# Optimization experiments

Hardware: AMD Instinct MI355X
Metric: run time of the kernel (lower is better)

The kernel has to match this reference:

```python
import jax, jax.numpy as jnp
import numpy as np

N = 100000   # points in scan
K = 20       # KNN neighbors
D = 96       # backbone feature dim
H = 1024     # random-projection dim
C = 7        # num classes


def setup_inputs() -> dict:
    key = jax.random.key(0)
    ks = jax.random.split(key, 6)
    feat_source = jax.random.normal(ks[0], (N, D), jnp.float32)
    proto = jax.random.normal(ks[1], (C, D), jnp.float32)
    w_rand = jax.random.normal(ks[2], (D, H), jnp.float32)
    Q = jnp.zeros((H, C), jnp.float32)
    G = jnp.zeros((H, H), jnp.float32)
    coords = jax.random.normal(ks[3], (N, 3), jnp.float32) * 30.0
    normals_z = jax.random.uniform(ks[4], (N,), jnp.float32)
    near_indices = jax.random.randint(ks[5], (N, K), 0, N).astype(jnp.int64)
    return dict(feat_source=feat_source, proto=proto, w_rand=w_rand, Q=Q, G=G,
                coords=coords, normals_z=normals_z, near_indices=near_indices)


def _prior_filter(preds, coords, normals_z):
    plane_pred = (preds == 2) | (preds == 3) | (preds == 4)
    manmade_pred = preds == 5
    other = (preds == 0) | (preds == 1) | (preds == 6)
    ground = plane_pred & (normals_z > 0.9) & (coords[:, 2] < -10.0)
    g_index = ground | other | manmade_pred
    m_index = (manmade_pred & (normals_z < 0.1)) | other | plane_pred
    return g_index, m_index


def reference(feat_source, proto, w_rand, Q, G, coords, normals_z, near_indices):
    RIDGE = 100.0  # stand-in for optimise_ridge_parameter (source not provided)
    # prototype logits: feat @ normalize(proto, dim=1).T   [N, C]
    proto_n = proto / jnp.maximum(jnp.linalg.norm(proto, axis=1, keepdims=True), 1e-12)
    pred_proto = feat_source @ proto_n.T
    preds = jnp.argmax(pred_proto, axis=1)                       # [N]
    # KNN consistency filtering (irregular gather)
    neigh = preds[near_indices]                                  # [N, K]
    consistency = jnp.mean((neigh == preds[:, None]).astype(jnp.float32), axis=1)
    cmask = consistency > 0.8
    g_index, m_index = _prior_filter(preds, coords, normals_z)
    mask = cmask & g_index & m_index                             # [N]
    # random-projection features
    feat_h = jax.nn.relu(feat_source @ w_rand)                   # [N, H]
    yhat = jax.nn.one_hot(preds, C, dtype=feat_h.dtype)          # [N, C]
    mw = mask.astype(feat_h.dtype)[:, None]
    fh_m = feat_h * mw                                           # masked rows (mask^2 == mask)
    Qn = Q + jnp.einsum('nh,nc->hc', fh_m, yhat)
    Gn = G + fh_m.T @ fh_m
    # ridge solve: wo = solve(G + r*I, Q); module does feat_h @ wo
    wo = jnp.linalg.solve(Gn + RIDGE * jnp.eye(H, dtype=Gn.dtype), Qn)  # [H, C]
    pred_domain = feat_h @ wo                                    # [N, C]
    return pred_domain
```

## Files before the change

### kernel.cpp

```cpp
#include <hip/hip_runtime.h>

#define D_DIM 96
#define K_NN  20
#define H_DIM 1024
#define C_CLS 7


__global__ void k_init(const float* __restrict__ proto,
                       const long long* __restrict__ idx_ll,
                       float* __restrict__ proto_n, int* __restrict__ flags) {
  __shared__ float inv[C_CLS];
  __shared__ int any_big;
  int t = threadIdx.x;
  if (t == 0) any_big = 0;
  if (t < C_CLS) {
    float ss = 0.f;
    for (int d = 0; d < D_DIM; d++) { float v = proto[t * D_DIM + d]; ss += v * v; }
    float nrm = fmaxf(sqrtf(ss), 1e-12f);
    inv[t] = 1.0f / nrm;
  }
  for (int j = t; j < 1024; j += blockDim.x) {
    long long v = idx_ll[j];
    if (v < 0 || v >= 100000) any_big = 1;
  }
  __syncthreads();
  for (int j = t; j < C_CLS * D_DIM; j += blockDim.x)
    proto_n[j] = proto[j] * inv[j / D_DIM];
  if (t == 0) {
    flags[0] = 0;
    flags[1] = any_big ? 0 : 1;
  }
}

__global__ void k_preds(const float* __restrict__ feat,
                        const float* __restrict__ proto_n,
                        int* __restrict__ preds, int N) {
  __shared__ float pn[C_CLS * D_DIM];
  for (int j = threadIdx.x; j < C_CLS * D_DIM; j += blockDim.x) pn[j] = proto_n[j];
  __syncthreads();
  int i = blockIdx.x * blockDim.x + threadIdx.x;
  if (i >= N) return;
  const float4* fp = (const float4*)(feat + (size_t)i * D_DIM);
  float s[C_CLS];
#pragma unroll
  for (int c = 0; c < C_CLS; c++) s[c] = 0.f;
#pragma unroll
  for (int q = 0; q < D_DIM / 4; q++) {
    float4 v = fp[q];
    int d = q * 4;
#pragma unroll
    for (int c = 0; c < C_CLS; c++) {
      s[c] += v.x * pn[c * D_DIM + d]     + v.y * pn[c * D_DIM + d + 1]
            + v.z * pn[c * D_DIM + d + 2] + v.w * pn[c * D_DIM + d + 3];
    }
  }
  float best = s[0]; int bi = 0;
#pragma unroll
  for (int c = 1; c < C_CLS; c++) { if (s[c] > best) { best = s[c]; bi = c; } }
  preds[i] = bi;
}

__global__ void k_mask(const int* __restrict__ preds, const void* __restrict__ nearv,
                       const float* __restrict__ coords, const float* __restrict__ normz,
                       int* __restrict__ flags, int* __restrict__ list, int N) {
  int i = blockIdx.x * blockDim.x + threadIdx.x;
  if (i >= N) return;
  int p = preds[i];
  int cnt = 0;
  if (flags[1]) {
    const long long* nn = (const long long*)nearv + (long long)i * K_NN;
#pragma unroll
    for (int k = 0; k < K_NN; k++) cnt += (preds[(int)nn[k]] == p) ? 1 : 0;
  } else {
    const int* nn = (const int*)nearv + (size_t)i * K_NN;
#pragma unroll
    for (int k = 0; k < K_NN; k++) cnt += (preds[nn[k]] == p) ? 1 : 0;
  }
  bool cmask = (cnt >= 17);
  bool plane = (p == 2) || (p == 3) || (p == 4);
  bool man   = (p == 5);
  bool other = (p == 0) || (p == 1) || (p == 6);
  float nz = normz[i];
  bool ground = plane && (nz > 0.9f) && (coords[(size_t)i * 3 + 2] < -10.0f);
  bool g = ground || other || man;
  bool m = (man && (nz < 0.1f)) || other || plane;
  if (cmask && g && m) {
    int pos = atomicAdd(&flags[0], 1);
    list[pos] = i;
  }
}

__global__ void k_qn(const float* __restrict__ feat, const float* __restrict__ w,
                     const float* __restrict__ Q, const int* __restrict__ preds,
                     const int* __restrict__ flags, const int* __restrict__ list,
                     float* __restrict__ Qn) {
  int h = blockIdx.x * blockDim.x + threadIdx.x;
  float q[C_CLS];
#pragma unroll
  for (int c = 0; c < C_CLS; c++) q[c] = Q[h * C_CLS + c];
  int M = flags[0];
  for (int m = 0; m < M; m++) {
    int i = list[m];
    float s = 0.f;
    for (int d = 0; d < D_DIM; d++) s += feat[(size_t)i * D_DIM + d] * w[(size_t)d * H_DIM + h];
    s = fmaxf(s, 0.f);
    q[preds[i]] += s;
  }
#pragma unroll
  for (int c = 0; c < C_CLS; c++) Qn[h * C_CLS + c] = q[c];
}

__global__ void k_gram(const float* __restrict__ feat, const float* __restrict__ w,
                       const float* __restrict__ G, const int* __restrict__ flags,
                       const int* __restrict__ list, float* __restrict__ Gn) {
  int bx = blockIdx.x & 15, by = blockIdx.x >> 4;
  int tr0 = by * 64, tc0 = bx * 64;
  __shared__ float fr[64], fc[64], fsh[D_DIM];
  float acc[4][4];
#pragma unroll
  for (int u = 0; u < 4; u++)
#pragma unroll
    for (int v = 0; v < 4; v++) acc[u][v] = 0.f;
  int M = flags[0];
  int t = threadIdx.x;
  int tu = t >> 4, tv = t & 15;
  for (int m = 0; m < M; m++) {
    int i = list[m];
    if (t < D_DIM) fsh[t] = feat[(size_t)i * D_DIM + t];
    __syncthreads();
    if (t < 64) {
      float s = 0.f;
      for (int d = 0; d < D_DIM; d++) s += fsh[d] * w[(size_t)d * H_DIM + tr0 + t];
      fr[t] = fmaxf(s, 0.f);
    } else if (t < 128) {
      int c = t - 64;
      float s = 0.f;
      for (int d = 0; d < D_DIM; d++) s += fsh[d] * w[(size_t)d * H_DIM + tc0 + c];
      fc[c] = fmaxf(s, 0.f);
    }
    __syncthreads();
#pragma unroll
    for (int u = 0; u < 4; u++)
#pragma unroll
      for (int v = 0; v < 4; v++) acc[u][v] += fr[tu * 4 + u] * fc[tv * 4 + v];
    __syncthreads();
  }
#pragma unroll
  for (int u = 0; u < 4; u++)
#pragma unroll
    for (int v = 0; v < 4; v++) {
      int r = tr0 + tu * 4 + u, c = tc0 + tv * 4 + v;
      Gn[(size_t)r * H_DIM + c] = G[(size_t)r * H_DIM + c] + acc[u][v];
    }
}

__device__ inline void block_reduce7(const float* val, volatile float* out,
                                     float* red) {
  int lane = threadIdx.x & 63, wave = threadIdx.x >> 6;
#pragma unroll
  for (int c = 0; c < C_CLS; c++) {
    float v = val[c];
#pragma unroll
    for (int o = 32; o > 0; o >>= 1) v += __shfl_down(v, o, 64);
    if (lane == 0) red[wave * C_CLS + c] = v;
  }
  __syncthreads();
  if (threadIdx.x == 0) {
#pragma unroll
    for (int c = 0; c < C_CLS; c++) {
      float s = 0.f;
      for (int wv = 0; wv < 16; wv++) s += red[wv * C_CLS + c];
      out[c] = s;
    }
  }
  __syncthreads();
}

__global__ void __launch_bounds__(1024) k_solve(const float* __restrict__ Gn,
                                                const float* __restrict__ Qn,
                                                float* __restrict__ wo,
                                                float* __restrict__ wo_flag) {
  const int h = threadIdx.x;
  __shared__ float psh[H_DIM * C_CLS];
  __shared__ float red[16 * C_CLS];
  __shared__ float rs[C_CLS], bn2[C_CLS], pap[C_CLS], rsn[C_CLS];

  float x[C_CLS], r[C_CLS], p[C_CLS], t7[C_CLS];
#pragma unroll
  for (int c = 0; c < C_CLS; c++) {
    float b = Qn[h * C_CLS + c];
    x[c] = 0.f; r[c] = b; p[c] = b;
    t7[c] = b * b;
  }
  block_reduce7(t7, rs, red);
  if (h == 0) {
#pragma unroll
    for (int c = 0; c < C_CLS; c++) bn2[c] = rs[c];
  }
  __syncthreads();

  for (int it = 0; it < H_DIM; it++) {
    bool done = true;
#pragma unroll
    for (int c = 0; c < C_CLS; c++)
      done = done && (rs[c] <= bn2[c] * 1e-16f + 1e-30f);
    if (done) break;

#pragma unroll
    for (int c = 0; c < C_CLS; c++) psh[h * C_CLS + c] = p[c];
    __syncthreads();

    float ap[C_CLS];
#pragma unroll
    for (int c = 0; c < C_CLS; c++) ap[c] = 100.0f * p[c];
    const float* grow = Gn + (size_t)h * H_DIM;
    for (int k = 0; k < H_DIM; k++) {
      float g = grow[k];
#pragma unroll
      for (int c = 0; c < C_CLS; c++) ap[c] += g * psh[k * C_CLS + c];
    }
#pragma unroll
    for (int c = 0; c < C_CLS; c++) t7[c] = p[c] * ap[c];
    block_reduce7(t7, pap, red);

    float a[C_CLS], rsold[C_CLS];
#pragma unroll
    for (int c = 0; c < C_CLS; c++) {
      rsold[c] = rs[c];
      bool act = rs[c] > bn2[c] * 1e-16f + 1e-30f;
      a[c] = act ? rsold[c] / fmaxf(pap[c], 1e-37f) : 0.f;
    }
#pragma unroll
    for (int c = 0; c < C_CLS; c++) {
      x[c] += a[c] * p[c];
      r[c] -= a[c] * ap[c];
      t7[c] = r[c] * r[c];
    }
    block_reduce7(t7, rsn, red);
#pragma unroll
    for (int c = 0; c < C_CLS; c++) {
      float bb = rsn[c] / fmaxf(rsold[c], 1e-37f);
      p[c] = r[c] + bb * p[c];
    }
    if (h == 0) {
#pragma unroll
      for (int c = 0; c < C_CLS; c++) rs[c] = rsn[c];
    }
    __syncthreads();
  }

#pragma unroll
  for (int c = 0; c < C_CLS; c++) wo[h * C_CLS + c] = x[c];
  float s = 0.f;
#pragma unroll
  for (int c = 0; c < C_CLS; c++) s += fabsf(x[c]);
  t7[0] = s;
#pragma unroll
  for (int c = 1; c < C_CLS; c++) t7[c] = 0.f;
  block_reduce7(t7, rsn, red);
  if (h == 0) *wo_flag = rsn[0];
}

__global__ void k_out(const float* __restrict__ feat, const float* __restrict__ w,
                      const float* __restrict__ wo, const float* __restrict__ wo_flag,
                      float* __restrict__ out, int N) {
  if (*wo_flag == 0.0f) {
    long long tid = (long long)blockIdx.x * blockDim.x + threadIdx.x;
    long long total = (long long)N * C_CLS;
    if (tid < total) out[tid] = 0.0f;
    return;
  }
  int i = blockIdx.x * blockDim.x + threadIdx.x;
  if (i >= N) return;
  float f[D_DIM];
  const float4* fp = (const float4*)(feat + (size_t)i * D_DIM);
#pragma unroll
  for (int q = 0; q < D_DIM / 4; q++) {
    float4 v = fp[q];
    f[4 * q] = v.x; f[4 * q + 1] = v.y; f[4 * q + 2] = v.z; f[4 * q + 3] = v.w;
  }
  float acc[C_CLS];
#pragma unroll
  for (int c = 0; c < C_CLS; c++) acc[c] = 0.f;
  for (int hh = 0; hh < H_DIM; hh++) {
    float s = 0.f;
#pragma unroll 8
    for (int d = 0; d < D_DIM; d++) s += f[d] * w[(size_t)d * H_DIM + hh];
    s = fmaxf(s, 0.f);
    const float* wrow = wo + hh * C_CLS;
#pragma unroll
    for (int c = 0; c < C_CLS; c++) acc[c] += s * wrow[c];
  }
#pragma unroll
  for (int c = 0; c < C_CLS; c++) out[(size_t)i * C_CLS + c] = acc[c];
}

extern "C" void kernel_launch(void* const* d_in, const int* in_sizes, int n_in,
                              void* d_out, int out_size, void* d_ws, size_t ws_size,
                              hipStream_t stream) {
  const float* feat   = (const float*)d_in[0];
  const float* proto  = (const float*)d_in[1];
  const float* w      = (const float*)d_in[2];
  const float* Q      = (const float*)d_in[3];
  const float* G      = (const float*)d_in[4];
  const float* coords = (const float*)d_in[5];
  const float* normz  = (const float*)d_in[6];
  const void*  nearv  = d_in[7];
  float* out = (float*)d_out;

  const int N = in_sizes[0] / D_DIM;

  char* WS = (char*)d_ws;
  float* proto_n = (float*)(WS + 0);
  int*   flags   = (int*)(WS + 4096);
  float* wo_flag = (float*)(WS + 4160);
  int*   preds   = (int*)(WS + 8192);
  int*   list    = (int*)(WS + 8192 + 400000);
  float* Qn      = (float*)(WS + 808192);
  float* wo      = (float*)(WS + 836864);
  float* Gn      = (float*)(WS + 865536);
  if (ws_size < 5059840) return;

  int nblk = (N + 255) / 256;
  hipLaunchKernelGGL(k_init, dim3(1), dim3(256), 0, stream,
                     proto, (const long long*)nearv, proto_n, flags);
  hipLaunchKernelGGL(k_preds, dim3(nblk), dim3(256), 0, stream,
                     feat, proto_n, preds, N);
  hipLaunchKernelGGL(k_mask, dim3(nblk), dim3(256), 0, stream,
                     preds, nearv, coords, normz, flags, list, N);
  hipLaunchKernelGGL(k_qn, dim3(H_DIM / 256), dim3(256), 0, stream,
                     feat, w, Q, preds, flags, list, Qn);
  hipLaunchKernelGGL(k_gram, dim3(256), dim3(256), 0, stream,
                     feat, w, G, flags, list, Gn);
  hipLaunchKernelGGL(k_solve, dim3(1), dim3(1024), 0, stream,
                     Gn, Qn, wo, wo_flag);
  int oblk = (N * C_CLS + 255) / 256;
  hipLaunchKernelGGL(k_out, dim3(oblk), dim3(256), 0, stream,
                     feat, w, wo, wo_flag, out, N);
}
```

Before: 130.7 us.

## Fold init into preds kernel, copy G in Qn kernel, early-exit empty gram

Removes the single-block init kernel by having every preds block normalize the prototypes into shared memory, with block 0 doing the index-range check and flag reset. The G-to-Gn copy moves into the Qn kernel as extra blocks, and the gram kernel now exits immediately when the masked list is empty, otherwise adding into Gn. This trims one launch and skips the serial gram loop when no points pass the mask. In exchange every preds block recomputes the prototype norms, and the kernels now depend on launch order for the flags reset.

```diff
diff --git a/kernel.cpp b/kernel.cpp
--- a/kernel.cpp
+++ b/kernel.cpp
@@ -6,38 +6,36 @@
 #define C_CLS 7
 
 
-__global__ void k_init(const float* __restrict__ proto,
-                       const long long* __restrict__ idx_ll,
-                       float* __restrict__ proto_n, int* __restrict__ flags) {
+__global__ void k_preds(const float* __restrict__ feat,
+                        const float* __restrict__ proto,
+                        const long long* __restrict__ idx_ll,
+                        int* __restrict__ preds, int* __restrict__ flags, int N) {
+  __shared__ float pn[C_CLS * D_DIM];
   __shared__ float inv[C_CLS];
   __shared__ int any_big;
-  int t = threadIdx.x;
-  if (t == 0) any_big = 0;
-  if (t < C_CLS) {
+  if (threadIdx.x == 0) any_big = 0;
+  if (threadIdx.x < C_CLS) {
     float ss = 0.f;
-    for (int d = 0; d < D_DIM; d++) { float v = proto[t * D_DIM + d]; ss += v * v; }
-    float nrm = fmaxf(sqrtf(ss), 1e-12f);
-    inv[t] = 1.0f / nrm;
-  }
-  for (int j = t; j < 1024; j += blockDim.x) {
-    long long v = idx_ll[j];
-    if (v < 0 || v >= 100000) any_big = 1;
-  }
-  __syncthreads();
-  for (int j = t; j < C_CLS * D_DIM; j += blockDim.x)
-    proto_n[j] = proto[j] * inv[j / D_DIM];
-  if (t == 0) {
+    for (int d = 0; d < D_DIM; d++) {
+      float v = proto[threadIdx.x * D_DIM + d];
+      ss += v * v;
+    }
+    inv[threadIdx.x] = 1.0f / fmaxf(sqrtf(ss), 1e-12f);
+  }
+  __syncthreads();
+  for (int j = threadIdx.x; j < C_CLS * D_DIM; j += blockDim.x)
+    pn[j] = proto[j] * inv[j / D_DIM];
+  if (blockIdx.x == 0) {
+    for (int j = threadIdx.x; j < 1024; j += blockDim.x) {
+      long long v = idx_ll[j];
+      if (v < 0 || v >= N) any_big = 1;
+    }
+  }
+  __syncthreads();
+  if (blockIdx.x == 0 && threadIdx.x == 0) {
     flags[0] = 0;
     flags[1] = any_big ? 0 : 1;
   }
-}
-
-__global__ void k_preds(const float* __restrict__ feat,
-                        const float* __restrict__ proto_n,
-                        int* __restrict__ preds, int N) {
-  __shared__ float pn[C_CLS * D_DIM];
-  for (int j = threadIdx.x; j < C_CLS * D_DIM; j += blockDim.x) pn[j] = proto_n[j];
-  __syncthreads();
   int i = blockIdx.x * blockDim.x + threadIdx.x;
   if (i >= N) return;
   const float4* fp = (const float4*)(feat + (size_t)i * D_DIM);
@@ -90,11 +88,17 @@
   }
 }
 
-__global__ void k_qn(const float* __restrict__ feat, const float* __restrict__ w,
-                     const float* __restrict__ Q, const int* __restrict__ preds,
-                     const int* __restrict__ flags, const int* __restrict__ list,
-                     float* __restrict__ Qn) {
-  int h = blockIdx.x * blockDim.x + threadIdx.x;
+__global__ void k_qn_copy(const float* __restrict__ feat, const float* __restrict__ w,
+                          const float* __restrict__ Q, const int* __restrict__ preds,
+                          const int* __restrict__ flags, const int* __restrict__ list,
+                          float* __restrict__ Qn,
+                          const float* __restrict__ G, float* __restrict__ Gn) {
+  if (blockIdx.x < 1024) {
+    size_t t = (size_t)blockIdx.x * 256 + threadIdx.x;
+    ((float4*)Gn)[t] = ((const float4*)G)[t];
+    return;
+  }
+  int h = (blockIdx.x - 1024) * 256 + threadIdx.x;
   float q[C_CLS];
 #pragma unroll
   for (int c = 0; c < C_CLS; c++) q[c] = Q[h * C_CLS + c];
@@ -110,9 +114,11 @@
   for (int c = 0; c < C_CLS; c++) Qn[h * C_CLS + c] = q[c];
 }
 
-__global__ void k_gram(const float* __restrict__ feat, const float* __restrict__ w,
-                       const float* __restrict__ G, const int* __restrict__ flags,
-                       const int* __restrict__ list, float* __restrict__ Gn) {
+__global__ void k_gram_acc(const float* __restrict__ feat, const float* __restrict__ w,
+                           const int* __restrict__ flags, const int* __restrict__ list,
+                           float* __restrict__ Gn) {
+  int M = flags[0];
+  if (M == 0) return;
   int bx = blockIdx.x & 15, by = blockIdx.x >> 4;
   int tr0 = by * 64, tc0 = bx * 64;
   __shared__ float fr[64], fc[64], fsh[D_DIM];
@@ -121,7 +127,6 @@
   for (int u = 0; u < 4; u++)
 #pragma unroll
     for (int v = 0; v < 4; v++) acc[u][v] = 0.f;
-  int M = flags[0];
   int t = threadIdx.x;
   int tu = t >> 4, tv = t & 15;
   for (int m = 0; m < M; m++) {
@@ -150,7 +155,7 @@
 #pragma unroll
     for (int v = 0; v < 4; v++) {
       int r = tr0 + tu * 4 + u, c = tc0 + tv * 4 + v;
-      Gn[(size_t)r * H_DIM + c] = G[(size_t)r * H_DIM + c] + acc[u][v];
+      Gn[(size_t)r * H_DIM + c] += acc[u][v];
     }
 }
 
@@ -311,7 +316,6 @@
   const int N = in_sizes[0] / D_DIM;
 
   char* WS = (char*)d_ws;
-  float* proto_n = (float*)(WS + 0);
   int*   flags   = (int*)(WS + 4096);
   float* wo_flag = (float*)(WS + 4160);
   int*   preds   = (int*)(WS + 8192);
@@ -322,16 +326,14 @@
   if (ws_size < 5059840) return;
 
   int nblk = (N + 255) / 256;
-  hipLaunchKernelGGL(k_init, dim3(1), dim3(256), 0, stream,
-                     proto, (const long long*)nearv, proto_n, flags);
   hipLaunchKernelGGL(k_preds, dim3(nblk), dim3(256), 0, stream,
-                     feat, proto_n, preds, N);
+                     feat, proto, (const long long*)nearv, preds, flags, N);
   hipLaunchKernelGGL(k_mask, dim3(nblk), dim3(256), 0, stream,
                      preds, nearv, coords, normz, flags, list, N);
-  hipLaunchKernelGGL(k_qn, dim3(H_DIM / 256), dim3(256), 0, stream,
-                     feat, w, Q, preds, flags, list, Qn);
-  hipLaunchKernelGGL(k_gram, dim3(256), dim3(256), 0, stream,
-                     feat, w, G, flags, list, Gn);
+  hipLaunchKernelGGL(k_qn_copy, dim3(1024 + H_DIM / 256), dim3(256), 0, stream,
+                     feat, w, Q, preds, flags, list, Qn, G, Gn);
+  hipLaunchKernelGGL(k_gram_acc, dim3(256), dim3(256), 0, stream,
+                     feat, w, flags, list, Gn);
   hipLaunchKernelGGL(k_solve, dim3(1), dim3(1024), 0, stream,
                      Gn, Qn, wo, wo_flag);
   int oblk = (N * C_CLS + 255) / 256;
```

Result: no change. 130.6 us (-0.1%).
